# Kernel tuning notes

Hardware: AMD Instinct MI355X
Metric: run time of the kernel (lower is better)

## Reference

```python
import jax, jax.numpy as jnp
import numpy as np

B, T, H, A = 64, 2048, 1024, 256

def setup_inputs() -> dict:
    key = jax.random.key(0)
    k1, k2, k3, k4 = jax.random.split(key, 4)
    inputs = jax.random.normal(k1, (B, T, H), dtype=jnp.float32)
    w_omega = jax.random.normal(k2, (H, A), dtype=jnp.float32) * 0.05
    b_omega = jax.random.normal(k3, (A,), dtype=jnp.float32) * 0.05
    u_omega = jax.random.normal(k4, (A,), dtype=jnp.float32) * 0.05
    return {"inputs": inputs, "w_omega": w_omega, "b_omega": b_omega, "u_omega": u_omega}

def reference(inputs, w_omega, b_omega, u_omega):
    # additive attention pooling: v = tanh(inputs @ w_omega + b_omega)  [B,T,A]
    v = jnp.tanh(jnp.einsum('bth,ha->bta', inputs, w_omega) + b_omega)
    # scores vu = <v, u_omega> over A, softmax over time dim T
    vu = jnp.einsum('bta,a->bt', v, u_omega)
    alphas = jax.nn.softmax(vu, axis=1)                      # [B,T]
    # weighted sum over time -> pooled [B,H]
    output = jnp.einsum('bth,bt->bh', inputs, alphas)
    # F.pad(x, (0,1), value=1) -> append constant-1 column
    embedding = jnp.pad(output, ((0, 0), (0, 1)), constant_values=1.0)  # [B,H+1]
    return embedding
```

## Files before the change

### kernel.cpp

```cpp
#include <hip/hip_runtime.h>

#define BB 64
#define TT 2048
#define HH 1024
#define AA 256
#define M_TILE 64
#define N_CHUNKS (TT / M_TILE)
#define NBLK (BB * TT / M_TILE)
#define KSTEPS (HH / 32)

typedef __attribute__((ext_vector_type(4))) float f32x4;
typedef __attribute__((ext_vector_type(8))) short s16x8;

__device__ __forceinline__ short f2bf(float f) {
    unsigned int u = __float_as_uint(f);
    u += 0x7fffu + ((u >> 16) & 1u);
    return (short)(u >> 16);
}

__device__ __forceinline__ float fast_tanh(float x) {
    x = fminf(fmaxf(x, -10.f), 10.f);
    float e = __expf(2.f * x);
    return (e - 1.f) / (e + 1.f);
}

__device__ __forceinline__ void gld_lds16(const void* gptr, void* lptr) {
    __builtin_amdgcn_global_load_lds(
        (const __attribute__((address_space(1))) unsigned int*)gptr,
        (__attribute__((address_space(3))) unsigned int*)lptr,
        16, 0, 0);
}

__global__ __launch_bounds__(256) void wconv_kernel(const float* __restrict__ w,
                                                    short* __restrict__ wfrag) {
    int t = blockIdx.x * 256 + threadIdx.x;
    int kq = t >> 8;
    int n  = t & 255;
    int kbase = kq * 8;
    s16x8 o;
#pragma unroll
    for (int j = 0; j < 8; ++j)
        o[j] = f2bf(w[(size_t)(kbase + j) * AA + n]);
    *(s16x8*)(wfrag + (size_t)t * 8) = o;
}

__global__ __launch_bounds__(256) void score_pool_kernel(
    const float* __restrict__ X,
    const short* __restrict__ wfrag,
    const float* __restrict__ bo,
    const float* __restrict__ uo,
    float* __restrict__ partials,
    float* __restrict__ mstats)
{
    __shared__ __attribute__((aligned(16))) short lds_a[M_TILE * 40];
    __shared__ __attribute__((aligned(16))) short lds_b[4 * 256 * 8];
    __shared__ float lds_red[4][M_TILE];
    __shared__ float lds_w[M_TILE];

    const int tid  = threadIdx.x;
    const int wave = tid >> 6;
    const int lane = tid & 63;
    const int q    = lane >> 4;
    const int ln   = lane & 15;
    const size_t m0 = (size_t)blockIdx.x * M_TILE;

    f32x4 acc[4][4];
    const f32x4 zero = {0.f, 0.f, 0.f, 0.f};
#pragma unroll
    for (int i = 0; i < 4; ++i)
#pragma unroll
        for (int j = 0; j < 4; ++j) acc[i][j] = zero;

    const int arow = tid >> 2;
    const int akp  = (tid & 3) * 8;
    const float* aptr = X + (m0 + (size_t)arow) * HH + akp;

    for (int kk = 0; kk < KSTEPS; ++kk) {
        if (kk) __syncthreads();
#pragma unroll
        for (int it = 0; it < 4; ++it) {
            int u = it * 256 + tid;
            gld_lds16(wfrag + (size_t)kk * 8192 + (size_t)u * 8, &lds_b[u * 8]);
        }
        const float4* ap = (const float4*)(aptr + kk * 32);
        float4 x0 = ap[0];
        float4 x1 = ap[1];
        s16x8 av;
        av[0] = f2bf(x0.x); av[1] = f2bf(x0.y); av[2] = f2bf(x0.z); av[3] = f2bf(x0.w);
        av[4] = f2bf(x1.x); av[5] = f2bf(x1.y); av[6] = f2bf(x1.z); av[7] = f2bf(x1.w);
        *(s16x8*)&lds_a[arow * 40 + akp] = av;
        __syncthreads();

        s16x8 af[4], bf[4];
#pragma unroll
        for (int mt = 0; mt < 4; ++mt)
            af[mt] = *(const s16x8*)&lds_a[(mt * 16 + ln) * 40 + q * 8];
#pragma unroll
        for (int nt = 0; nt < 4; ++nt)
            bf[nt] = *(const s16x8*)&lds_b[q * 2048 + (wave * 64 + nt * 16 + ln) * 8];
#pragma unroll
        for (int mt = 0; mt < 4; ++mt)
#pragma unroll
            for (int nt = 0; nt < 4; ++nt)
                acc[mt][nt] = __builtin_amdgcn_mfma_f32_16x16x32_bf16(
                    af[mt], bf[nt], acc[mt][nt], 0, 0, 0);
    }

    float bv[4], uv[4];
#pragma unroll
    for (int nt = 0; nt < 4; ++nt) {
        int n = wave * 64 + nt * 16 + ln;
        bv[nt] = bo[n];
        uv[nt] = uo[n];
    }
    float s[4][4];
#pragma unroll
    for (int mt = 0; mt < 4; ++mt) {
#pragma unroll
        for (int r = 0; r < 4; ++r) {
            float v = 0.f;
#pragma unroll
            for (int nt = 0; nt < 4; ++nt) {
                float p = acc[mt][nt][r] + bv[nt];
                v += fast_tanh(p) * uv[nt];
            }
            v += __shfl_xor(v, 1);
            v += __shfl_xor(v, 2);
            v += __shfl_xor(v, 4);
            v += __shfl_xor(v, 8);
            s[mt][r] = v;
        }
    }
    if (ln == 0) {
#pragma unroll
        for (int mt = 0; mt < 4; ++mt)
#pragma unroll
            for (int r = 0; r < 4; ++r)
                lds_red[wave][mt * 16 + q * 4 + r] = s[mt][r];
    }
    __syncthreads();

    if (tid < 64) {
        float sv = lds_red[0][tid] + lds_red[1][tid] + lds_red[2][tid] + lds_red[3][tid];
        float mx = sv;
        mx = fmaxf(mx, __shfl_xor(mx, 1));
        mx = fmaxf(mx, __shfl_xor(mx, 2));
        mx = fmaxf(mx, __shfl_xor(mx, 4));
        mx = fmaxf(mx, __shfl_xor(mx, 8));
        mx = fmaxf(mx, __shfl_xor(mx, 16));
        mx = fmaxf(mx, __shfl_xor(mx, 32));
        float wv = __expf(sv - mx);
        float ls = wv;
        ls += __shfl_xor(ls, 1);
        ls += __shfl_xor(ls, 2);
        ls += __shfl_xor(ls, 4);
        ls += __shfl_xor(ls, 8);
        ls += __shfl_xor(ls, 16);
        ls += __shfl_xor(ls, 32);
        lds_w[tid] = wv;
        if (tid == 0) {
            mstats[2 * blockIdx.x]     = mx;
            mstats[2 * blockIdx.x + 1] = ls;
        }
    }
    __syncthreads();

    float4 o = {0.f, 0.f, 0.f, 0.f};
    const float* xb = X + m0 * HH + tid * 4;
#pragma unroll 4
    for (int t = 0; t < M_TILE; ++t) {
        float wt = lds_w[t];
        float4 xv = *(const float4*)(xb + (size_t)t * HH);
        o.x += wt * xv.x;
        o.y += wt * xv.y;
        o.z += wt * xv.z;
        o.w += wt * xv.w;
    }
    *(float4*)(partials + (size_t)blockIdx.x * HH + tid * 4) = o;
}

__global__ __launch_bounds__(256) void combine_kernel(
    const float* __restrict__ partials,
    const float* __restrict__ mstats,
    float* __restrict__ out)
{
    int b = blockIdx.x;
    int tid = threadIdx.x;
    float M = -1e30f;
#pragma unroll
    for (int c = 0; c < N_CHUNKS; ++c)
        M = fmaxf(M, mstats[2 * (b * N_CHUNKS + c)]);
    float denom = 0.f;
    float4 o = {0.f, 0.f, 0.f, 0.f};
    for (int c = 0; c < N_CHUNKS; ++c) {
        int ch = b * N_CHUNKS + c;
        float sc = __expf(mstats[2 * ch] - M);
        denom += sc * mstats[2 * ch + 1];
        float4 p = *(const float4*)(partials + (size_t)ch * HH + tid * 4);
        o.x += sc * p.x;
        o.y += sc * p.y;
        o.z += sc * p.z;
        o.w += sc * p.w;
    }
    float inv = 1.f / denom;
    float* orow = out + (size_t)b * (HH + 1) + tid * 4;
    orow[0] = o.x * inv;
    orow[1] = o.y * inv;
    orow[2] = o.z * inv;
    orow[3] = o.w * inv;
    if (tid == 0) out[(size_t)b * (HH + 1) + HH] = 1.0f;
}

extern "C" void kernel_launch(void* const* d_in, const int* in_sizes, int n_in,
                              void* d_out, int out_size, void* d_ws, size_t ws_size,
                              hipStream_t stream) {
    const float* X  = (const float*)d_in[0];
    const float* w  = (const float*)d_in[1];
    const float* bo = (const float*)d_in[2];
    const float* uo = (const float*)d_in[3];
    float* out = (float*)d_out;

    char* ws = (char*)d_ws;
    short* wfrag    = (short*)ws;
    float* partials = (float*)(ws + (512u << 10));
    float* mstats   = (float*)(ws + (512u << 10) + (8u << 20));

    wconv_kernel<<<128, 256, 0, stream>>>(w, wfrag);
    score_pool_kernel<<<NBLK, 256, 0, stream>>>(X, wfrag, bo, uo, partials, mstats);
    combine_kernel<<<BB, 256, 0, stream>>>(partials, mstats, out);
}
```

Baseline: 784.8 us.

## Stage whole bf16 X tile in LDS and reuse it for pooling

The score kernel now loads a full 32-row by 1024 slice of X into LDS as bf16 in one pass. It then runs the K loop without per-step barriers, prefetching A fragments from LDS and B fragments straight from global memory into registers. The weighted time-pooling reads that bf16 LDS copy instead of reading X from global a second time, which removes the duplicate X traffic. The costs are that pooling now uses bf16-rounded activations, each block makes several times more global/L2 reads of the weight fragments, and the large LDS footprint limits how many blocks fit on a CU. Block size goes to 512 threads with half the rows per block, and the partials buffer offset doubles to match.

```diff
diff --git a/kernel.cpp b/kernel.cpp
--- a/kernel.cpp
+++ b/kernel.cpp
@@ -4,13 +4,15 @@
 #define TT 2048
 #define HH 1024
 #define AA 256
-#define M_TILE 64
+#define M_TILE 32
 #define N_CHUNKS (TT / M_TILE)
 #define NBLK (BB * TT / M_TILE)
 #define KSTEPS (HH / 32)
+#define LDA 1032
 
 typedef __attribute__((ext_vector_type(4))) float f32x4;
 typedef __attribute__((ext_vector_type(8))) short s16x8;
+typedef __attribute__((ext_vector_type(4))) short s16x4;
 
 __device__ __forceinline__ short f2bf(float f) {
     unsigned int u = __float_as_uint(f);
@@ -18,17 +20,14 @@
     return (short)(u >> 16);
 }
 
+__device__ __forceinline__ float bf2f(unsigned short u) {
+    return __uint_as_float((unsigned int)u << 16);
+}
+
 __device__ __forceinline__ float fast_tanh(float x) {
     x = fminf(fmaxf(x, -10.f), 10.f);
     float e = __expf(2.f * x);
     return (e - 1.f) / (e + 1.f);
-}
-
-__device__ __forceinline__ void gld_lds16(const void* gptr, void* lptr) {
-    __builtin_amdgcn_global_load_lds(
-        (const __attribute__((address_space(1))) unsigned int*)gptr,
-        (__attribute__((address_space(3))) unsigned int*)lptr,
-        16, 0, 0);
 }
 
 __global__ __launch_bounds__(256) void wconv_kernel(const float* __restrict__ w,
@@ -44,7 +43,7 @@
     *(s16x8*)(wfrag + (size_t)t * 8) = o;
 }
 
-__global__ __launch_bounds__(256) void score_pool_kernel(
+__global__ __launch_bounds__(512, 4) void score_pool_kernel(
     const float* __restrict__ X,
     const short* __restrict__ wfrag,
     const float* __restrict__ bo,
@@ -52,8 +51,7 @@
     float* __restrict__ partials,
     float* __restrict__ mstats)
 {
-    __shared__ __attribute__((aligned(16))) short lds_a[M_TILE * 40];
-    __shared__ __attribute__((aligned(16))) short lds_b[4 * 256 * 8];
+    __shared__ __attribute__((aligned(16))) short ldsA[M_TILE * LDA];
     __shared__ float lds_red[4][M_TILE];
     __shared__ float lds_w[M_TILE];
 
@@ -62,85 +60,80 @@
     const int lane = tid & 63;
     const int q    = lane >> 4;
     const int ln   = lane & 15;
+    const int wm   = wave >> 2;
+    const int wn   = wave & 3;
     const size_t m0 = (size_t)blockIdx.x * M_TILE;
 
-    f32x4 acc[4][4];
+    const float4* xt = (const float4*)(X + m0 * HH);
+#pragma unroll
+    for (int j = 0; j < 16; ++j) {
+        int f = j * 512 + tid;
+        float4 v = xt[f];
+        int row = f >> 8;
+        int c4  = f & 255;
+        s16x4 pk;
+        pk[0] = f2bf(v.x); pk[1] = f2bf(v.y); pk[2] = f2bf(v.z); pk[3] = f2bf(v.w);
+        *(s16x4*)&ldsA[row * LDA + c4 * 4] = pk;
+    }
+    __syncthreads();
+
+    f32x4 acc[4];
     const f32x4 zero = {0.f, 0.f, 0.f, 0.f};
 #pragma unroll
-    for (int i = 0; i < 4; ++i)
-#pragma unroll
-        for (int j = 0; j < 4; ++j) acc[i][j] = zero;
-
-    const int arow = tid >> 2;
-    const int akp  = (tid & 3) * 8;
-    const float* aptr = X + (m0 + (size_t)arow) * HH + akp;
-
-    for (int kk = 0; kk < KSTEPS; ++kk) {
-        if (kk) __syncthreads();
-#pragma unroll
-        for (int it = 0; it < 4; ++it) {
-            int u = it * 256 + tid;
-            gld_lds16(wfrag + (size_t)kk * 8192 + (size_t)u * 8, &lds_b[u * 8]);
+    for (int nt = 0; nt < 4; ++nt) acc[nt] = zero;
+
+    const int arow_off = (wm * 16 + ln) * LDA + q * 8;
+    const size_t bbase = (size_t)q * 2048;
+
+    s16x8 a_cur = *(const s16x8*)&ldsA[arow_off];
+    s16x8 b_cur[4];
+#pragma unroll
+    for (int nt = 0; nt < 4; ++nt) {
+        int n = wn * 64 + nt * 16 + ln;
+        b_cur[nt] = *(const s16x8*)(wfrag + bbase + (size_t)n * 8);
+    }
+
+    for (int kk = 0; kk < KSTEPS - 1; ++kk) {
+        s16x8 a_nxt = *(const s16x8*)&ldsA[arow_off + (kk + 1) * 32];
+        s16x8 b_nxt[4];
+#pragma unroll
+        for (int nt = 0; nt < 4; ++nt) {
+            int n = wn * 64 + nt * 16 + ln;
+            b_nxt[nt] = *(const s16x8*)(wfrag + (size_t)(kk + 1) * 8192 + bbase + (size_t)n * 8);
         }
-        const float4* ap = (const float4*)(aptr + kk * 32);
-        float4 x0 = ap[0];
-        float4 x1 = ap[1];
-        s16x8 av;
-        av[0] = f2bf(x0.x); av[1] = f2bf(x0.y); av[2] = f2bf(x0.z); av[3] = f2bf(x0.w);
-        av[4] = f2bf(x1.x); av[5] = f2bf(x1.y); av[6] = f2bf(x1.z); av[7] = f2bf(x1.w);
-        *(s16x8*)&lds_a[arow * 40 + akp] = av;
-        __syncthreads();
-
-        s16x8 af[4], bf[4];
-#pragma unroll
-        for (int mt = 0; mt < 4; ++mt)
-            af[mt] = *(const s16x8*)&lds_a[(mt * 16 + ln) * 40 + q * 8];
 #pragma unroll
         for (int nt = 0; nt < 4; ++nt)
-            bf[nt] = *(const s16x8*)&lds_b[q * 2048 + (wave * 64 + nt * 16 + ln) * 8];
-#pragma unroll
-        for (int mt = 0; mt < 4; ++mt)
-#pragma unroll
-            for (int nt = 0; nt < 4; ++nt)
-                acc[mt][nt] = __builtin_amdgcn_mfma_f32_16x16x32_bf16(
-                    af[mt], bf[nt], acc[mt][nt], 0, 0, 0);
-    }
+            acc[nt] = __builtin_amdgcn_mfma_f32_16x16x32_bf16(a_cur, b_cur[nt], acc[nt], 0, 0, 0);
+        a_cur = a_nxt;
+#pragma unroll
+        for (int nt = 0; nt < 4; ++nt) b_cur[nt] = b_nxt[nt];
+    }
+#pragma unroll
+    for (int nt = 0; nt < 4; ++nt)
+        acc[nt] = __builtin_amdgcn_mfma_f32_16x16x32_bf16(a_cur, b_cur[nt], acc[nt], 0, 0, 0);
 
     float bv[4], uv[4];
 #pragma unroll
     for (int nt = 0; nt < 4; ++nt) {
-        int n = wave * 64 + nt * 16 + ln;
+        int n = wn * 64 + nt * 16 + ln;
         bv[nt] = bo[n];
         uv[nt] = uo[n];
     }
-    float s[4][4];
-#pragma unroll
-    for (int mt = 0; mt < 4; ++mt) {
-#pragma unroll
-        for (int r = 0; r < 4; ++r) {
-            float v = 0.f;
-#pragma unroll
-            for (int nt = 0; nt < 4; ++nt) {
-                float p = acc[mt][nt][r] + bv[nt];
-                v += fast_tanh(p) * uv[nt];
-            }
-            v += __shfl_xor(v, 1);
-            v += __shfl_xor(v, 2);
-            v += __shfl_xor(v, 4);
-            v += __shfl_xor(v, 8);
-            s[mt][r] = v;
-        }
-    }
-    if (ln == 0) {
-#pragma unroll
-        for (int mt = 0; mt < 4; ++mt)
-#pragma unroll
-            for (int r = 0; r < 4; ++r)
-                lds_red[wave][mt * 16 + q * 4 + r] = s[mt][r];
+#pragma unroll
+    for (int r = 0; r < 4; ++r) {
+        float v = 0.f;
+#pragma unroll
+        for (int nt = 0; nt < 4; ++nt)
+            v += fast_tanh(acc[nt][r] + bv[nt]) * uv[nt];
+        v += __shfl_xor(v, 1);
+        v += __shfl_xor(v, 2);
+        v += __shfl_xor(v, 4);
+        v += __shfl_xor(v, 8);
+        if (ln == 0) lds_red[wn][wm * 16 + q * 4 + r] = v;
     }
     __syncthreads();
 
-    if (tid < 64) {
+    if (tid < M_TILE) {
         float sv = lds_red[0][tid] + lds_red[1][tid] + lds_red[2][tid] + lds_red[3][tid];
         float mx = sv;
         mx = fmaxf(mx, __shfl_xor(mx, 1));
@@ -148,7 +141,6 @@
         mx = fmaxf(mx, __shfl_xor(mx, 4));
         mx = fmaxf(mx, __shfl_xor(mx, 8));
         mx = fmaxf(mx, __shfl_xor(mx, 16));
-        mx = fmaxf(mx, __shfl_xor(mx, 32));
         float wv = __expf(sv - mx);
         float ls = wv;
         ls += __shfl_xor(ls, 1);
@@ -156,7 +148,6 @@
         ls += __shfl_xor(ls, 4);
         ls += __shfl_xor(ls, 8);
         ls += __shfl_xor(ls, 16);
-        ls += __shfl_xor(ls, 32);
         lds_w[tid] = wv;
         if (tid == 0) {
             mstats[2 * blockIdx.x]     = mx;
@@ -165,18 +156,17 @@
     }
     __syncthreads();
 
-    float4 o = {0.f, 0.f, 0.f, 0.f};
-    const float* xb = X + m0 * HH + tid * 4;
-#pragma unroll 4
+    float ox = 0.f, oy = 0.f;
+    const int cbyte = tid * 4;
+#pragma unroll 8
     for (int t = 0; t < M_TILE; ++t) {
         float wt = lds_w[t];
-        float4 xv = *(const float4*)(xb + (size_t)t * HH);
-        o.x += wt * xv.x;
-        o.y += wt * xv.y;
-        o.z += wt * xv.z;
-        o.w += wt * xv.w;
-    }
-    *(float4*)(partials + (size_t)blockIdx.x * HH + tid * 4) = o;
+        unsigned int pk = *(const unsigned int*)((const char*)ldsA + (size_t)t * (LDA * 2) + cbyte);
+        ox += wt * bf2f((unsigned short)(pk & 0xffffu));
+        oy += wt * bf2f((unsigned short)(pk >> 16));
+    }
+    float2 o2 = {ox, oy};
+    *(float2*)(partials + (size_t)blockIdx.x * HH + tid * 2) = o2;
 }
 
 __global__ __launch_bounds__(256) void combine_kernel(
@@ -192,6 +182,7 @@
         M = fmaxf(M, mstats[2 * (b * N_CHUNKS + c)]);
     float denom = 0.f;
     float4 o = {0.f, 0.f, 0.f, 0.f};
+#pragma unroll 4
     for (int c = 0; c < N_CHUNKS; ++c) {
         int ch = b * N_CHUNKS + c;
         float sc = __expf(mstats[2 * ch] - M);
@@ -223,9 +214,9 @@
     char* ws = (char*)d_ws;
     short* wfrag    = (short*)ws;
     float* partials = (float*)(ws + (512u << 10));
-    float* mstats   = (float*)(ws + (512u << 10) + (8u << 20));
+    float* mstats   = (float*)(ws + (512u << 10) + (16u << 20));
 
     wconv_kernel<<<128, 256, 0, stream>>>(w, wfrag);
-    score_pool_kernel<<<NBLK, 256, 0, stream>>>(X, wfrag, bo, uo, partials, mstats);
+    score_pool_kernel<<<NBLK, 512, 0, stream>>>(X, wfrag, bo, uo, partials, mstats);
     combine_kernel<<<BB, 256, 0, stream>>>(partials, mstats, out);
 }
```

Measured after the change: 795.5 us. Within noise of the previous version (+1.4%).
